# Optimization experiments

Measured on AMD Instinct MI355X. Metric: run time of the kernel, lower is better.

Reference implementation:

```python
import jax, jax.numpy as jnp
import numpy as np
import math

B, SQ, SKV, D = 16, 1024, 1024, 256


def setup_inputs() -> dict:
    key = jax.random.key(0)
    kq, kk, kv, km = jax.random.split(key, 4)
    # Scale inputs down: the module applies exp() to raw QK^T logits, so dot
    # products must stay small to avoid overflow (std ~ 0.05^2*sqrt(D) ~ 0.04).
    scale = 0.05
    query = jax.random.normal(kq, (B, SQ, D), dtype=jnp.float32) * scale
    key_t = jax.random.normal(kk, (B, SKV, D), dtype=jnp.float32) * scale
    value = jax.random.normal(kv, (B, SKV, D), dtype=jnp.float32)
    mask = jax.random.randint(km, (B, SQ, SKV), 0, 2, dtype=jnp.int32)
    return {"query": query, "key": key_t, "value": value, "mask": mask}


def reference(query, key, value, mask):
    # scores = exp(Q K^T) / sqrt(d)  -- note: exp BEFORE scaling, as in source
    d = query.shape[-1]
    inv_sqrt_d = jnp.float32(1.0 / math.sqrt(d))
    scores = jnp.exp(jnp.einsum('bqd,bkd->bqk', query, key)) * inv_sqrt_d
    # masked_fill(mask == 0, -1e9)
    scores = jnp.where(mask == 0, jnp.float32(-1e9), scores)
    p_attn = jax.nn.softmax(scores, axis=-1)
    # dropout is identity in eval mode (deterministic reference)
    output = jnp.einsum('bqk,bkd->bqd', p_attn, value)
    # flatten=True path: sum over the query/sequence dim
    return output.sum(axis=1), p_attn
```

## Files before the change

### kernel.cpp

```cpp
#include <hip/hip_runtime.h>

#define NB   16
#define NSQ  1024
#define NSKV 1024
#define ND   256

typedef __bf16    bf16x8 __attribute__((ext_vector_type(8)));
typedef float     f32x4  __attribute__((ext_vector_type(4)));
typedef _Float16  f16x4  __attribute__((ext_vector_type(4)));

#define EST 268

__global__ __launch_bounds__(256) void prep_kernel(
    const float* __restrict__ K, __bf16* __restrict__ Kbf,
    const int* __restrict__ mask, unsigned* __restrict__ mw,
    float* __restrict__ colsum, float* __restrict__ out0)
{
    const int bid = blockIdx.x;
    const int tid = threadIdx.x;
    if (bid < 2048) {
        const int i    = bid * 256 + tid;
        const int lane = i & 63;
        const int m    = lane & 15;
        const int kg   = lane >> 4;
        const int dc   = (i >> 6) & 7;
        const int kvb  = (i >> 9) & 63;
        const int b    = i >> 15;
        const float* s = K + ((size_t)(b * NSKV + kvb * 16 + m)) * ND + dc * 32 + kg * 8;
        float4 a = *(const float4*)s;
        float4 c = *(const float4*)(s + 4);
        bf16x8 o;
        o[0] = (__bf16)a.x; o[1] = (__bf16)a.y; o[2] = (__bf16)a.z; o[3] = (__bf16)a.w;
        o[4] = (__bf16)c.x; o[5] = (__bf16)c.y; o[6] = (__bf16)c.z; o[7] = (__bf16)c.w;
        ((bf16x8*)Kbf)[i] = o;
    } else if (bid < 2048 + 4096) {
        const int row = (bid - 2048) * 4 + (tid >> 6);
        const int l   = tid & 63;
        const int4* mrow = (const int4*)(mask + (size_t)row * NSKV) + l * 4;
        unsigned w = 0;
        #pragma unroll
        for (int v = 0; v < 4; ++v) {
            int4 mv = mrow[v];
            w |= (mv.x != 0 ? 1u : 0u) << (v * 4 + 0);
            w |= (mv.y != 0 ? 1u : 0u) << (v * 4 + 1);
            w |= (mv.z != 0 ? 1u : 0u) << (v * 4 + 2);
            w |= (mv.w != 0 ? 1u : 0u) << (v * 4 + 3);
        }
        const int m    = l & 15;
        const int base = l & 48;
        unsigned out = 0;
        #pragma unroll
        for (int c = 0; c < 16; ++c) {
            unsigned v = (unsigned)__shfl((int)w, base | c);
            out |= ((v >> m) & 1u) << c;
        }
        mw[(size_t)row * 64 + l] = out;
    } else if (bid < 2048 + 4096 + 64) {
        colsum[(bid - 6144) * 256 + tid] = 0.f;
    } else {
        out0[(bid - 6208) * 256 + tid] = 0.f;
    }
}

__global__ __launch_bounds__(256, 4) void attn_fused(
    const float* __restrict__ Q, const __bf16* __restrict__ Kbf,
    const unsigned* __restrict__ mw, float* __restrict__ out_p,
    float* __restrict__ colsum)
{
    const int b    = blockIdx.x >> 6;
    const int qt   = blockIdx.x & 63;
    const int q0   = qt * 16;
    const int tid  = threadIdx.x;
    const int lane = tid & 63;
    const int h    = tid >> 6;
    const int m    = lane & 15;
    const int kg   = lane >> 4;

    __shared__ __attribute__((aligned(16))) _Float16 epark[4][16 * EST];
    __shared__ float Zs[4][16];
    __shared__ float invZs[16];

    _Float16* myE = &epark[h][0];

    bf16x8 afrag[8];
    {
        const float* qbase = Q + ((size_t)(b * NSQ + q0 + m)) * ND;
        #pragma unroll
        for (int dc = 0; dc < 8; ++dc) {
            const float* p4 = qbase + dc * 32 + kg * 8;
            float4 x = *(const float4*)(p4);
            float4 y = *(const float4*)(p4 + 4);
            bf16x8 a;
            a[0] = (__bf16)x.x; a[1] = (__bf16)x.y; a[2] = (__bf16)x.z; a[3] = (__bf16)x.w;
            a[4] = (__bf16)y.x; a[5] = (__bf16)y.y; a[6] = (__bf16)y.z; a[7] = (__bf16)y.w;
            afrag[dc] = a;
        }
    }

    unsigned mword[4];
    #pragma unroll
    for (int i = 0; i < 4; ++i)
        mword[i] = mw[(size_t)(b * NSQ + q0 + kg * 4 + i) * 64 + h * 16 + m];

    const bf16x8* kf = (const bf16x8*)Kbf + ((size_t)(b * 64 + h * 16) * 8) * 64 + lane;

    float zacc[4] = {0.f, 0.f, 0.f, 0.f};
    bf16x8 fA[8], fB[8];

    #define LDFRAG(g, c) { \
        _Pragma("unroll") \
        for (int dc = 0; dc < 8; ++dc) \
            (g)[dc] = kf[((c) * 8 + dc) * 64]; }

    #define COMPUTE(g, c) { \
        f32x4 acc = {0.f, 0.f, 0.f, 0.f}; \
        _Pragma("unroll") \
        for (int dc = 0; dc < 8; ++dc) \
            acc = __builtin_amdgcn_mfma_f32_16x16x32_bf16(afrag[dc], (g)[dc], acc, 0, 0, 0); \
        _Pragma("unroll") \
        for (int i = 0; i < 4; ++i) { \
            float e = ((mword[i] >> (c)) & 1u) ? __expf(__expf(acc[i]) * 0.0625f) : 0.f; \
            zacc[i] += e; \
            myE[(kg * 4 + i) * EST + (c) * 16 + m] = (_Float16)e; \
        } }

    LDFRAG(fA, 0);

    #pragma unroll
    for (int cc = 0; cc < 16; cc += 2) {
        LDFRAG(fB, cc + 1);
        COMPUTE(fA, cc);
        if (cc + 2 < 16) LDFRAG(fA, cc + 2);
        COMPUTE(fB, cc + 1);
    }

    #pragma unroll
    for (int i = 0; i < 4; ++i) {
        float z = zacc[i];
        z += __shfl_xor(z, 1);
        z += __shfl_xor(z, 2);
        z += __shfl_xor(z, 4);
        z += __shfl_xor(z, 8);
        if (m == 0) Zs[h][kg * 4 + i] = z;
    }
    __syncthreads();
    if (tid < 16)
        invZs[tid] = 1.0f / (Zs[0][tid] + Zs[1][tid] + Zs[2][tid] + Zs[3][tid]);
    __syncthreads();

    float csum[4] = {0.f, 0.f, 0.f, 0.f};
    float* prow = out_p + (size_t)(b * NSQ + q0) * NSKV + h * 256 + lane * 4;
    #pragma unroll
    for (int s = 0; s < 16; ++s) {
        f16x4 ev = *(const f16x4*)&myE[s * EST + lane * 4];
        const float iz = invZs[s];
        float4 pv;
        pv.x = (float)ev[0] * iz; pv.y = (float)ev[1] * iz;
        pv.z = (float)ev[2] * iz; pv.w = (float)ev[3] * iz;
        *(float4*)(prow + (size_t)s * NSKV) = pv;
        csum[0] += pv.x; csum[1] += pv.y; csum[2] += pv.z; csum[3] += pv.w;
    }
    #pragma unroll
    for (int j = 0; j < 4; ++j)
        atomicAdd(&colsum[b * NSKV + h * 256 + lane * 4 + j], csum[j]);

    #undef LDFRAG
    #undef COMPUTE
}

__global__ __launch_bounds__(256) void attn_out_kernel(
    const float* __restrict__ colsum, const float* __restrict__ V,
    float* __restrict__ out)
{
    const int b  = blockIdx.x >> 6;
    const int ks = (blockIdx.x & 63) << 4;
    const int d  = threadIdx.x;
    float acc = 0.f;
    #pragma unroll
    for (int k = 0; k < 16; ++k) {
        acc += colsum[b * NSKV + ks + k] * V[((size_t)(b * NSKV + ks + k)) * ND + d];
    }
    atomicAdd(&out[b * ND + d], acc);
}

extern "C" void kernel_launch(void* const* d_in, const int* in_sizes, int n_in,
                              void* d_out, int out_size, void* d_ws, size_t ws_size,
                              hipStream_t stream)
{
    (void)in_sizes; (void)n_in; (void)out_size; (void)ws_size;
    const float* Q    = (const float*)d_in[0];
    const float* K    = (const float*)d_in[1];
    const float* V    = (const float*)d_in[2];
    const int*   mask = (const int*)d_in[3];

    float* out0 = (float*)d_out;
    float* p    = out0 + NB * ND;

    float*    colsum = (float*)d_ws;
    __bf16*   Kbf    = (__bf16*)((char*)d_ws + (64 << 10));
    unsigned* mwbits = (unsigned*)((char*)d_ws + (64 << 10) + (size_t)NB * NSKV * ND * 2);

    prep_kernel<<<6224, 256, 0, stream>>>(K, Kbf, mask, mwbits, colsum, out0);
    attn_fused<<<NB * 64, 256, 0, stream>>>(Q, Kbf, mwbits, p, colsum);
    attn_out_kernel<<<NB * 64, 256, 0, stream>>>(colsum, V, out0);
}
```

Baseline: 204.3 us.

## Make attention kernel persistent with LDS DMA K loads and deferred P stores

The fused attention kernel now runs 512 blocks that each process two query tiles. K fragments are streamed into double-buffered LDS through global_load_lds DMA, paced by explicit vmcnt waits. The previous tile's P rows are held in registers and written out interleaved with the next tile's DMA, so the global stores overlap compute. This aims to hide the K load latency and the large P write traffic, at the cost of higher register pressure (occupancy hint drops from 4 to 2 blocks) and fragile hand-written waitcnt ordering.

```diff
diff --git a/kernel.cpp b/kernel.cpp
--- a/kernel.cpp
+++ b/kernel.cpp
@@ -62,109 +62,149 @@
     }
 }
 
-__global__ __launch_bounds__(256, 4) void attn_fused(
+__device__ __forceinline__ void gload_lds16(const void* g, void* l) {
+    __builtin_amdgcn_global_load_lds(
+        (const __attribute__((address_space(1))) void*)g,
+        (__attribute__((address_space(3))) void*)l, 16, 0, 0);
+}
+
+__global__ __launch_bounds__(256, 2) void attn_fused(
     const float* __restrict__ Q, const __bf16* __restrict__ Kbf,
     const unsigned* __restrict__ mw, float* __restrict__ out_p,
     float* __restrict__ colsum)
 {
-    const int b    = blockIdx.x >> 6;
-    const int qt   = blockIdx.x & 63;
-    const int q0   = qt * 16;
     const int tid  = threadIdx.x;
     const int lane = tid & 63;
     const int h    = tid >> 6;
     const int m    = lane & 15;
     const int kg   = lane >> 4;
 
-    __shared__ __attribute__((aligned(16))) _Float16 epark[4][16 * EST];
+    __shared__ __attribute__((aligned(16))) char kbuf[4][2][8192];
     __shared__ float Zs[4][16];
     __shared__ float invZs[16];
 
-    _Float16* myE = &epark[h][0];
-
-    bf16x8 afrag[8];
-    {
-        const float* qbase = Q + ((size_t)(b * NSQ + q0 + m)) * ND;
-        #pragma unroll
-        for (int dc = 0; dc < 8; ++dc) {
-            const float* p4 = qbase + dc * 32 + kg * 8;
-            float4 x = *(const float4*)(p4);
-            float4 y = *(const float4*)(p4 + 4);
-            bf16x8 a;
-            a[0] = (__bf16)x.x; a[1] = (__bf16)x.y; a[2] = (__bf16)x.z; a[3] = (__bf16)x.w;
-            a[4] = (__bf16)y.x; a[5] = (__bf16)y.y; a[6] = (__bf16)y.z; a[7] = (__bf16)y.w;
-            afrag[dc] = a;
-        }
-    }
-
-    unsigned mword[4];
-    #pragma unroll
-    for (int i = 0; i < 4; ++i)
-        mword[i] = mw[(size_t)(b * NSQ + q0 + kg * 4 + i) * 64 + h * 16 + m];
-
-    const bf16x8* kf = (const bf16x8*)Kbf + ((size_t)(b * 64 + h * 16) * 8) * 64 + lane;
-
-    float zacc[4] = {0.f, 0.f, 0.f, 0.f};
-    bf16x8 fA[8], fB[8];
-
-    #define LDFRAG(g, c) { \
+    char* buf0 = &kbuf[h][0][0];
+    char* buf1 = &kbuf[h][1][0];
+    _Float16* myE = (_Float16*)buf0;
+
+    float4 pregs[16];
+    float* prow_prev = nullptr;
+
+    #define WAITVM(N) { asm volatile("s_waitcnt vmcnt(" #N ")" ::: "memory"); \
+                        __builtin_amdgcn_sched_barrier(0); }
+
+    #define DMA(bufp, c) { \
+        const char* _g = kf0 + (size_t)(c) * 8192; \
         _Pragma("unroll") \
-        for (int dc = 0; dc < 8; ++dc) \
-            (g)[dc] = kf[((c) * 8 + dc) * 64]; }
-
-    #define COMPUTE(g, c) { \
+        for (int j = 0; j < 8; ++j) \
+            gload_lds16(_g + j * 1024, (bufp) + j * 1024); }
+
+    #define COMPUTE(bufp, c) { \
         f32x4 acc = {0.f, 0.f, 0.f, 0.f}; \
         _Pragma("unroll") \
-        for (int dc = 0; dc < 8; ++dc) \
-            acc = __builtin_amdgcn_mfma_f32_16x16x32_bf16(afrag[dc], (g)[dc], acc, 0, 0, 0); \
+        for (int j = 0; j < 8; ++j) { \
+            bf16x8 bfr = *(const bf16x8*)((bufp) + j * 1024 + lane * 16); \
+            acc = __builtin_amdgcn_mfma_f32_16x16x32_bf16(afrag[j], bfr, acc, 0, 0, 0); \
+        } \
         _Pragma("unroll") \
         for (int i = 0; i < 4; ++i) { \
             float e = ((mword[i] >> (c)) & 1u) ? __expf(__expf(acc[i]) * 0.0625f) : 0.f; \
             zacc[i] += e; \
-            myE[(kg * 4 + i) * EST + (c) * 16 + m] = (_Float16)e; \
+            ebuf[c][i] = (_Float16)e; \
         } }
 
-    LDFRAG(fA, 0);
+    for (int t = 0; t < 2; ++t) {
+        const int tile = (int)blockIdx.x + t * 512;
+        const int b    = tile >> 6;
+        const int q0   = (tile & 63) * 16;
+        const bool prev = (t != 0);
+
+        bf16x8 afrag[8];
+        {
+            const float* qbase = Q + ((size_t)(b * NSQ + q0 + m)) * ND;
+            #pragma unroll
+            for (int dc = 0; dc < 8; ++dc) {
+                const float* p4 = qbase + dc * 32 + kg * 8;
+                float4 x = *(const float4*)(p4);
+                float4 y = *(const float4*)(p4 + 4);
+                bf16x8 a;
+                a[0] = (__bf16)x.x; a[1] = (__bf16)x.y; a[2] = (__bf16)x.z; a[3] = (__bf16)x.w;
+                a[4] = (__bf16)y.x; a[5] = (__bf16)y.y; a[6] = (__bf16)y.z; a[7] = (__bf16)y.w;
+                afrag[dc] = a;
+            }
+        }
+
+        unsigned mword[4];
+        #pragma unroll
+        for (int i = 0; i < 4; ++i)
+            mword[i] = mw[(size_t)(b * NSQ + q0 + kg * 4 + i) * 64 + h * 16 + m];
+
+        const char* kf0 = (const char*)Kbf
+                        + ((size_t)(b * 64 + h * 16) * 8 * 64) * 16 + lane * 16;
+
+        float zacc[4] = {0.f, 0.f, 0.f, 0.f};
+        f16x4 ebuf[16];
+
+        if (prev) *(float4*)(prow_prev + (size_t)0 * NSKV) = pregs[0];
+        DMA(buf0, 0);
+        if (prev) *(float4*)(prow_prev + (size_t)1 * NSKV) = pregs[1];
+        DMA(buf1, 1);
+
+        #pragma unroll
+        for (int cc = 0; cc < 16; ++cc) {
+            if (cc < 15) { WAITVM(8); } else { WAITVM(0); }
+            char* cbuf = (cc & 1) ? buf1 : buf0;
+            COMPUTE(cbuf, cc);
+            if (cc < 14) {
+                if (prev) *(float4*)(prow_prev + (size_t)(cc + 2) * NSKV) = pregs[cc + 2];
+                DMA(cbuf, cc + 2);
+            }
+        }
+
+        #pragma unroll
+        for (int c = 0; c < 16; ++c)
+            #pragma unroll
+            for (int i = 0; i < 4; ++i)
+                myE[(kg * 4 + i) * EST + c * 16 + m] = ebuf[c][i];
+
+        #pragma unroll
+        for (int i = 0; i < 4; ++i) {
+            float z = zacc[i];
+            z += __shfl_xor(z, 1);
+            z += __shfl_xor(z, 2);
+            z += __shfl_xor(z, 4);
+            z += __shfl_xor(z, 8);
+            if (m == 0) Zs[h][kg * 4 + i] = z;
+        }
+        __syncthreads();
+        if (tid < 16)
+            invZs[tid] = 1.0f / (Zs[0][tid] + Zs[1][tid] + Zs[2][tid] + Zs[3][tid]);
+        __syncthreads();
+
+        float csum[4] = {0.f, 0.f, 0.f, 0.f};
+        #pragma unroll
+        for (int s = 0; s < 16; ++s) {
+            f16x4 ev = *(const f16x4*)&myE[s * EST + lane * 4];
+            const float iz = invZs[s];
+            float4 pv;
+            pv.x = (float)ev[0] * iz; pv.y = (float)ev[1] * iz;
+            pv.z = (float)ev[2] * iz; pv.w = (float)ev[3] * iz;
+            pregs[s] = pv;
+            csum[0] += pv.x; csum[1] += pv.y; csum[2] += pv.z; csum[3] += pv.w;
+        }
+        #pragma unroll
+        for (int j = 0; j < 4; ++j)
+            atomicAdd(&colsum[b * NSKV + h * 256 + lane * 4 + j], csum[j]);
+
+        prow_prev = out_p + (size_t)(b * NSQ + q0) * NSKV + h * 256 + lane * 4;
+    }
 
     #pragma unroll
-    for (int cc = 0; cc < 16; cc += 2) {
-        LDFRAG(fB, cc + 1);
-        COMPUTE(fA, cc);
-        if (cc + 2 < 16) LDFRAG(fA, cc + 2);
-        COMPUTE(fB, cc + 1);
-    }
-
-    #pragma unroll
-    for (int i = 0; i < 4; ++i) {
-        float z = zacc[i];
-        z += __shfl_xor(z, 1);
-        z += __shfl_xor(z, 2);
-        z += __shfl_xor(z, 4);
-        z += __shfl_xor(z, 8);
-        if (m == 0) Zs[h][kg * 4 + i] = z;
-    }
-    __syncthreads();
-    if (tid < 16)
-        invZs[tid] = 1.0f / (Zs[0][tid] + Zs[1][tid] + Zs[2][tid] + Zs[3][tid]);
-    __syncthreads();
-
-    float csum[4] = {0.f, 0.f, 0.f, 0.f};
-    float* prow = out_p + (size_t)(b * NSQ + q0) * NSKV + h * 256 + lane * 4;
-    #pragma unroll
-    for (int s = 0; s < 16; ++s) {
-        f16x4 ev = *(const f16x4*)&myE[s * EST + lane * 4];
-        const float iz = invZs[s];
-        float4 pv;
-        pv.x = (float)ev[0] * iz; pv.y = (float)ev[1] * iz;
-        pv.z = (float)ev[2] * iz; pv.w = (float)ev[3] * iz;
-        *(float4*)(prow + (size_t)s * NSKV) = pv;
-        csum[0] += pv.x; csum[1] += pv.y; csum[2] += pv.z; csum[3] += pv.w;
-    }
-    #pragma unroll
-    for (int j = 0; j < 4; ++j)
-        atomicAdd(&colsum[b * NSKV + h * 256 + lane * 4 + j], csum[j]);
-
-    #undef LDFRAG
+    for (int s = 0; s < 16; ++s)
+        *(float4*)(prow_prev + (size_t)s * NSKV) = pregs[s];
+
+    #undef WAITVM
+    #undef DMA
     #undef COMPUTE
 }
 
@@ -201,6 +241,6 @@
     unsigned* mwbits = (unsigned*)((char*)d_ws + (64 << 10) + (size_t)NB * NSKV * ND * 2);
 
     prep_kernel<<<6224, 256, 0, stream>>>(K, Kbf, mask, mwbits, colsum, out0);
-    attn_fused<<<NB * 64, 256, 0, stream>>>(Q, Kbf, mwbits, p, colsum);
+    attn_fused<<<512, 256, 0, stream>>>(Q, Kbf, mwbits, p, colsum);
     attn_out_kernel<<<NB * 64, 256, 0, stream>>>(colsum, V, out0);
 }
```

Result: no change. 202.8 us (-0.7%).

## Split fused attention into a normalizer pass and a recompute-and-write pass

Applied to the files above, without the earlier changes.

The fused kernel is replaced by two kernels. The first computes only the row normalizers 1/Z and writes them to workspace. The second recomputes QK^T and the double exponential, then writes normalized probabilities straight from registers, with the column sums reduced by shuffles and atomics. This removes the large shared-memory staging buffer, which raises occupancy and drops the fp16 round-trip, and it adds a blockIdx swizzle meant to improve L2 locality. In exchange the MFMA and exp work runs twice, and the p stores become strided 4-byte scalar writes instead of float4 rows.

```diff
diff --git a/kernel.cpp b/kernel.cpp
--- a/kernel.cpp
+++ b/kernel.cpp
@@ -7,9 +7,6 @@
 
 typedef __bf16    bf16x8 __attribute__((ext_vector_type(8)));
 typedef float     f32x4  __attribute__((ext_vector_type(4)));
-typedef _Float16  f16x4  __attribute__((ext_vector_type(4)));
-
-#define EST 268
 
 __global__ __launch_bounds__(256) void prep_kernel(
     const float* __restrict__ K, __bf16* __restrict__ Kbf,
@@ -62,25 +59,21 @@
     }
 }
 
-__global__ __launch_bounds__(256, 4) void attn_fused(
+__global__ __launch_bounds__(256) void zed_kernel(
     const float* __restrict__ Q, const __bf16* __restrict__ Kbf,
-    const unsigned* __restrict__ mw, float* __restrict__ out_p,
-    float* __restrict__ colsum)
-{
-    const int b    = blockIdx.x >> 6;
-    const int qt   = blockIdx.x & 63;
-    const int q0   = qt * 16;
+    const unsigned* __restrict__ mw, float* __restrict__ invZ)
+{
+    const int g    = blockIdx.x;
+    const int tile = ((g & 7) << 7) | (g >> 3);
+    const int b    = tile >> 6;
+    const int q0   = (tile & 63) * 16;
     const int tid  = threadIdx.x;
     const int lane = tid & 63;
     const int h    = tid >> 6;
     const int m    = lane & 15;
     const int kg   = lane >> 4;
 
-    __shared__ __attribute__((aligned(16))) _Float16 epark[4][16 * EST];
     __shared__ float Zs[4][16];
-    __shared__ float invZs[16];
-
-    _Float16* myE = &epark[h][0];
 
     bf16x8 afrag[8];
     {
@@ -107,32 +100,32 @@
     float zacc[4] = {0.f, 0.f, 0.f, 0.f};
     bf16x8 fA[8], fB[8];
 
-    #define LDFRAG(g, c) { \
-        _Pragma("unroll") \
-        for (int dc = 0; dc < 8; ++dc) \
-            (g)[dc] = kf[((c) * 8 + dc) * 64]; }
-
-    #define COMPUTE(g, c) { \
+    #define LDFRAG(gr, c) { \
+        _Pragma("unroll") \
+        for (int dc = 0; dc < 8; ++dc) \
+            (gr)[dc] = kf[((c) * 8 + dc) * 64]; }
+
+    #define ZCOMP(gr, c) { \
         f32x4 acc = {0.f, 0.f, 0.f, 0.f}; \
         _Pragma("unroll") \
         for (int dc = 0; dc < 8; ++dc) \
-            acc = __builtin_amdgcn_mfma_f32_16x16x32_bf16(afrag[dc], (g)[dc], acc, 0, 0, 0); \
+            acc = __builtin_amdgcn_mfma_f32_16x16x32_bf16(afrag[dc], (gr)[dc], acc, 0, 0, 0); \
         _Pragma("unroll") \
         for (int i = 0; i < 4; ++i) { \
             float e = ((mword[i] >> (c)) & 1u) ? __expf(__expf(acc[i]) * 0.0625f) : 0.f; \
             zacc[i] += e; \
-            myE[(kg * 4 + i) * EST + (c) * 16 + m] = (_Float16)e; \
         } }
 
     LDFRAG(fA, 0);
-
     #pragma unroll
     for (int cc = 0; cc < 16; cc += 2) {
         LDFRAG(fB, cc + 1);
-        COMPUTE(fA, cc);
+        ZCOMP(fA, cc);
         if (cc + 2 < 16) LDFRAG(fA, cc + 2);
-        COMPUTE(fB, cc + 1);
-    }
+        ZCOMP(fB, cc + 1);
+    }
+    #undef LDFRAG
+    #undef ZCOMP
 
     #pragma unroll
     for (int i = 0; i < 4; ++i) {
@@ -145,27 +138,85 @@
     }
     __syncthreads();
     if (tid < 16)
-        invZs[tid] = 1.0f / (Zs[0][tid] + Zs[1][tid] + Zs[2][tid] + Zs[3][tid]);
-    __syncthreads();
-
-    float csum[4] = {0.f, 0.f, 0.f, 0.f};
-    float* prow = out_p + (size_t)(b * NSQ + q0) * NSKV + h * 256 + lane * 4;
-    #pragma unroll
-    for (int s = 0; s < 16; ++s) {
-        f16x4 ev = *(const f16x4*)&myE[s * EST + lane * 4];
-        const float iz = invZs[s];
-        float4 pv;
-        pv.x = (float)ev[0] * iz; pv.y = (float)ev[1] * iz;
-        pv.z = (float)ev[2] * iz; pv.w = (float)ev[3] * iz;
-        *(float4*)(prow + (size_t)s * NSKV) = pv;
-        csum[0] += pv.x; csum[1] += pv.y; csum[2] += pv.z; csum[3] += pv.w;
-    }
-    #pragma unroll
-    for (int j = 0; j < 4; ++j)
-        atomicAdd(&colsum[b * NSKV + h * 256 + lane * 4 + j], csum[j]);
-
+        invZ[b * NSQ + q0 + tid] = 1.0f / (Zs[0][tid] + Zs[1][tid] + Zs[2][tid] + Zs[3][tid]);
+}
+
+__global__ __launch_bounds__(256) void p_kernel(
+    const float* __restrict__ Q, const __bf16* __restrict__ Kbf,
+    const unsigned* __restrict__ mw, const float* __restrict__ invZ,
+    float* __restrict__ out_p, float* __restrict__ colsum)
+{
+    const int g    = blockIdx.x;
+    const int tile = ((g & 7) << 7) | (g >> 3);
+    const int b    = tile >> 6;
+    const int q0   = (tile & 63) * 16;
+    const int tid  = threadIdx.x;
+    const int lane = tid & 63;
+    const int h    = tid >> 6;
+    const int m    = lane & 15;
+    const int kg   = lane >> 4;
+
+    bf16x8 afrag[8];
+    {
+        const float* qbase = Q + ((size_t)(b * NSQ + q0 + m)) * ND;
+        #pragma unroll
+        for (int dc = 0; dc < 8; ++dc) {
+            const float* p4 = qbase + dc * 32 + kg * 8;
+            float4 x = *(const float4*)(p4);
+            float4 y = *(const float4*)(p4 + 4);
+            bf16x8 a;
+            a[0] = (__bf16)x.x; a[1] = (__bf16)x.y; a[2] = (__bf16)x.z; a[3] = (__bf16)x.w;
+            a[4] = (__bf16)y.x; a[5] = (__bf16)y.y; a[6] = (__bf16)y.z; a[7] = (__bf16)y.w;
+            afrag[dc] = a;
+        }
+    }
+
+    unsigned mword[4];
+    float    iz[4];
+    #pragma unroll
+    for (int i = 0; i < 4; ++i) {
+        mword[i] = mw[(size_t)(b * NSQ + q0 + kg * 4 + i) * 64 + h * 16 + m];
+        iz[i]    = invZ[b * NSQ + q0 + kg * 4 + i];
+    }
+
+    const bf16x8* kf = (const bf16x8*)Kbf + ((size_t)(b * 64 + h * 16) * 8) * 64 + lane;
+    float* pbase = out_p + (size_t)(b * NSQ + q0) * NSKV + h * 256 + m;
+    float* cbase = colsum + b * NSKV + h * 256 + m;
+
+    bf16x8 fA[8], fB[8];
+
+    #define LDFRAG(gr, c) { \
+        _Pragma("unroll") \
+        for (int dc = 0; dc < 8; ++dc) \
+            (gr)[dc] = kf[((c) * 8 + dc) * 64]; }
+
+    #define PCOMP(gr, c) { \
+        f32x4 acc = {0.f, 0.f, 0.f, 0.f}; \
+        _Pragma("unroll") \
+        for (int dc = 0; dc < 8; ++dc) \
+            acc = __builtin_amdgcn_mfma_f32_16x16x32_bf16(afrag[dc], (gr)[dc], acc, 0, 0, 0); \
+        float cs = 0.f; \
+        _Pragma("unroll") \
+        for (int i = 0; i < 4; ++i) { \
+            float e  = ((mword[i] >> (c)) & 1u) ? __expf(__expf(acc[i]) * 0.0625f) : 0.f; \
+            float pv = e * iz[i]; \
+            pbase[(size_t)(kg * 4 + i) * NSKV + (c) * 16] = pv; \
+            cs += pv; \
+        } \
+        cs += __shfl_xor(cs, 16); \
+        cs += __shfl_xor(cs, 32); \
+        if (kg == 0) atomicAdd(cbase + (c) * 16, cs); }
+
+    LDFRAG(fA, 0);
+    #pragma unroll
+    for (int cc = 0; cc < 16; cc += 2) {
+        LDFRAG(fB, cc + 1);
+        PCOMP(fA, cc);
+        if (cc + 2 < 16) LDFRAG(fA, cc + 2);
+        PCOMP(fB, cc + 1);
+    }
     #undef LDFRAG
-    #undef COMPUTE
+    #undef PCOMP
 }
 
 __global__ __launch_bounds__(256) void attn_out_kernel(
@@ -197,10 +248,12 @@
     float* p    = out0 + NB * ND;
 
     float*    colsum = (float*)d_ws;
-    __bf16*   Kbf    = (__bf16*)((char*)d_ws + (64 << 10));
-    unsigned* mwbits = (unsigned*)((char*)d_ws + (64 << 10) + (size_t)NB * NSKV * ND * 2);
+    float*    invZ   = (float*)((char*)d_ws + (64 << 10));
+    __bf16*   Kbf    = (__bf16*)((char*)d_ws + (128 << 10));
+    unsigned* mwbits = (unsigned*)((char*)d_ws + (128 << 10) + (size_t)NB * NSKV * ND * 2);
 
     prep_kernel<<<6224, 256, 0, stream>>>(K, Kbf, mask, mwbits, colsum, out0);
-    attn_fused<<<NB * 64, 256, 0, stream>>>(Q, Kbf, mwbits, p, colsum);
+    zed_kernel<<<NB * 64, 256, 0, stream>>>(Q, Kbf, mwbits, invZ);
+    p_kernel<<<NB * 64, 256, 0, stream>>>(Q, Kbf, mwbits, invZ, p, colsum);
     attn_out_kernel<<<NB * 64, 256, 0, stream>>>(colsum, V, out0);
 }
```

Measured after the change: 218.8 us. +7.1%, slower.

## Split attention into two-pass normalizer and probability kernels with LDS-staged K

Applied to the files above, without the earlier changes.

Replaces the single fused kernel, which parked f16 exp values in LDS and normalized afterward, with two kernels. The first computes only the row normalizers and writes 1/Z to workspace. The second recomputes QK^T and exp and writes normalized probabilities directly, with colsum atomics reduced across lanes first. Both stream K tiles into double-buffered LDS via global_load_lds DMA, with each workgroup covering 64 query rows so K is reused across more rows. This removes the f16 parking step and its LDS traffic, at the cost of doing the MFMA and exp work twice and launching fewer, larger blocks (256).

```diff
diff --git a/kernel.cpp b/kernel.cpp
--- a/kernel.cpp
+++ b/kernel.cpp
@@ -7,9 +7,6 @@
 
 typedef __bf16    bf16x8 __attribute__((ext_vector_type(8)));
 typedef float     f32x4  __attribute__((ext_vector_type(4)));
-typedef _Float16  f16x4  __attribute__((ext_vector_type(4)));
-
-#define EST 268
 
 __global__ __launch_bounds__(256) void prep_kernel(
     const float* __restrict__ K, __bf16* __restrict__ Kbf,
@@ -62,77 +59,101 @@
     }
 }
 
-__global__ __launch_bounds__(256, 4) void attn_fused(
+__device__ __forceinline__ void gload_lds16(const void* g, void* l) {
+    __builtin_amdgcn_global_load_lds(
+        (const __attribute__((address_space(1))) void*)g,
+        (__attribute__((address_space(3))) void*)l, 16, 0, 0);
+}
+
+
+#define PROLOGUE_COMMON \
+    const int g    = blockIdx.x; \
+    const int tile = ((g & 7) << 5) | (g >> 3); \
+    const int b    = tile >> 4; \
+    const int q0   = (tile & 15) * 64; \
+    const int tid  = threadIdx.x; \
+    const int lane = tid & 63; \
+    const int h    = tid >> 6; \
+    const int m    = lane & 15; \
+    const int kg   = lane >> 4; \
+    const int r0   = q0 + h * 16; \
+    bf16x8 afrag[8]; \
+    { \
+        const float* qbase = Q + ((size_t)(b * NSQ + r0 + m)) * ND; \
+        _Pragma("unroll") \
+        for (int dc = 0; dc < 8; ++dc) { \
+            const float* p4 = qbase + dc * 32 + kg * 8; \
+            float4 x = *(const float4*)(p4); \
+            float4 y = *(const float4*)(p4 + 4); \
+            bf16x8 a; \
+            a[0] = (__bf16)x.x; a[1] = (__bf16)x.y; a[2] = (__bf16)x.z; a[3] = (__bf16)x.w; \
+            a[4] = (__bf16)y.x; a[5] = (__bf16)y.y; a[6] = (__bf16)y.z; a[7] = (__bf16)y.w; \
+            afrag[dc] = a; \
+        } \
+    } \
+    unsigned long long mbits[4]; \
+    _Pragma("unroll") \
+    for (int i = 0; i < 4; ++i) { \
+        const unsigned* wp = mw + (size_t)(b * NSQ + r0 + kg * 4 + i) * 64 + m; \
+        unsigned long long w0 = wp[0], w1 = wp[16], w2 = wp[32], w3 = wp[48]; \
+        mbits[i] = w0 | (w1 << 16) | (w2 << 32) | (w3 << 48); \
+    } \
+    const char* ksrc = (const char*)Kbf + (size_t)b * 64 * 512 * 16; \
+    const int soff = h * 8192 + lane * 16; \
+    const int doff = h * 8192;
+
+#define DMA(c, dst) { \
+    const char* _g = ksrc + (size_t)(c) * 32768 + soff; \
+    char* _l = (dst) + doff; \
+    _Pragma("unroll") \
+    for (int j = 0; j < 8; ++j) \
+        gload_lds16(_g + j * 1024, _l + j * 1024); }
+
+#define SYNC(N) { asm volatile("s_waitcnt vmcnt(" #N ")" ::: "memory"); \
+                  __builtin_amdgcn_s_barrier(); \
+                  __builtin_amdgcn_sched_barrier(0); }
+
+__global__ __launch_bounds__(256) void zk_kernel(
     const float* __restrict__ Q, const __bf16* __restrict__ Kbf,
-    const unsigned* __restrict__ mw, float* __restrict__ out_p,
-    float* __restrict__ colsum)
-{
-    const int b    = blockIdx.x >> 6;
-    const int qt   = blockIdx.x & 63;
-    const int q0   = qt * 16;
-    const int tid  = threadIdx.x;
-    const int lane = tid & 63;
-    const int h    = tid >> 6;
-    const int m    = lane & 15;
-    const int kg   = lane >> 4;
-
-    __shared__ __attribute__((aligned(16))) _Float16 epark[4][16 * EST];
-    __shared__ float Zs[4][16];
-    __shared__ float invZs[16];
-
-    _Float16* myE = &epark[h][0];
-
-    bf16x8 afrag[8];
-    {
-        const float* qbase = Q + ((size_t)(b * NSQ + q0 + m)) * ND;
-        #pragma unroll
-        for (int dc = 0; dc < 8; ++dc) {
-            const float* p4 = qbase + dc * 32 + kg * 8;
-            float4 x = *(const float4*)(p4);
-            float4 y = *(const float4*)(p4 + 4);
-            bf16x8 a;
-            a[0] = (__bf16)x.x; a[1] = (__bf16)x.y; a[2] = (__bf16)x.z; a[3] = (__bf16)x.w;
-            a[4] = (__bf16)y.x; a[5] = (__bf16)y.y; a[6] = (__bf16)y.z; a[7] = (__bf16)y.w;
-            afrag[dc] = a;
-        }
-    }
-
-    unsigned mword[4];
-    #pragma unroll
-    for (int i = 0; i < 4; ++i)
-        mword[i] = mw[(size_t)(b * NSQ + q0 + kg * 4 + i) * 64 + h * 16 + m];
-
-    const bf16x8* kf = (const bf16x8*)Kbf + ((size_t)(b * 64 + h * 16) * 8) * 64 + lane;
-
+    const unsigned* __restrict__ mw, float* __restrict__ invZ)
+{
+    __shared__ __attribute__((aligned(16))) char kst[2][32768];
+    PROLOGUE_COMMON
+    char* b0 = &kst[0][0];
+    char* b1 = &kst[1][0];
     float zacc[4] = {0.f, 0.f, 0.f, 0.f};
-    bf16x8 fA[8], fB[8];
-
-    #define LDFRAG(g, c) { \
+
+    #define ZCOMP(cb, c) { \
         _Pragma("unroll") \
-        for (int dc = 0; dc < 8; ++dc) \
-            (g)[dc] = kf[((c) * 8 + dc) * 64]; }
-
-    #define COMPUTE(g, c) { \
-        f32x4 acc = {0.f, 0.f, 0.f, 0.f}; \
-        _Pragma("unroll") \
-        for (int dc = 0; dc < 8; ++dc) \
-            acc = __builtin_amdgcn_mfma_f32_16x16x32_bf16(afrag[dc], (g)[dc], acc, 0, 0, 0); \
-        _Pragma("unroll") \
-        for (int i = 0; i < 4; ++i) { \
-            float e = ((mword[i] >> (c)) & 1u) ? __expf(__expf(acc[i]) * 0.0625f) : 0.f; \
-            zacc[i] += e; \
-            myE[(kg * 4 + i) * EST + (c) * 16 + m] = (_Float16)e; \
+        for (int cs = 0; cs < 4; ++cs) { \
+            f32x4 acc = {0.f, 0.f, 0.f, 0.f}; \
+            _Pragma("unroll") \
+            for (int dc = 0; dc < 8; ++dc) { \
+                bf16x8 bfr = *(const bf16x8*)((cb) + cs * 8192 + dc * 1024 + lane * 16); \
+                acc = __builtin_amdgcn_mfma_f32_16x16x32_bf16(afrag[dc], bfr, acc, 0, 0, 0); \
+            } \
+            const int C_ = (c) * 4 + cs; \
+            _Pragma("unroll") \
+            for (int i = 0; i < 4; ++i) { \
+                float e = ((mbits[i] >> C_) & 1ull) ? __expf(__expf(acc[i]) * 0.0625f) : 0.f; \
+                zacc[i] += e; \
+            } \
         } }
 
-    LDFRAG(fA, 0);
-
-    #pragma unroll
-    for (int cc = 0; cc < 16; cc += 2) {
-        LDFRAG(fB, cc + 1);
-        COMPUTE(fA, cc);
-        if (cc + 2 < 16) LDFRAG(fA, cc + 2);
-        COMPUTE(fB, cc + 1);
-    }
+    DMA(0, b0);
+    SYNC(0);
+    DMA(1, b1);
+    for (int c = 0; c < 16; c += 2) {
+        ZCOMP(b0, c);
+        SYNC(0);
+        if (c + 2 < 16) DMA(c + 2, b0);
+        ZCOMP(b1, c + 1);
+        if (c + 2 < 16) {
+            SYNC(0);
+            DMA(c + 3, b1);
+        }
+    }
+    #undef ZCOMP
 
     #pragma unroll
     for (int i = 0; i < 4; ++i) {
@@ -141,31 +162,65 @@
         z += __shfl_xor(z, 2);
         z += __shfl_xor(z, 4);
         z += __shfl_xor(z, 8);
-        if (m == 0) Zs[h][kg * 4 + i] = z;
-    }
-    __syncthreads();
-    if (tid < 16)
-        invZs[tid] = 1.0f / (Zs[0][tid] + Zs[1][tid] + Zs[2][tid] + Zs[3][tid]);
-    __syncthreads();
-
-    float csum[4] = {0.f, 0.f, 0.f, 0.f};
-    float* prow = out_p + (size_t)(b * NSQ + q0) * NSKV + h * 256 + lane * 4;
+        if (m == 0) invZ[b * NSQ + r0 + kg * 4 + i] = 1.0f / z;
+    }
+}
+
+__global__ __launch_bounds__(256) void pk_kernel(
+    const float* __restrict__ Q, const __bf16* __restrict__ Kbf,
+    const unsigned* __restrict__ mw, const float* __restrict__ invZ,
+    float* __restrict__ out_p, float* __restrict__ colsum)
+{
+    __shared__ __attribute__((aligned(16))) char kst[2][32768];
+    PROLOGUE_COMMON
+    char* b0 = &kst[0][0];
+    char* b1 = &kst[1][0];
+
+    float iz[4];
     #pragma unroll
-    for (int s = 0; s < 16; ++s) {
-        f16x4 ev = *(const f16x4*)&myE[s * EST + lane * 4];
-        const float iz = invZs[s];
-        float4 pv;
-        pv.x = (float)ev[0] * iz; pv.y = (float)ev[1] * iz;
-        pv.z = (float)ev[2] * iz; pv.w = (float)ev[3] * iz;
-        *(float4*)(prow + (size_t)s * NSKV) = pv;
-        csum[0] += pv.x; csum[1] += pv.y; csum[2] += pv.z; csum[3] += pv.w;
-    }
-    #pragma unroll
-    for (int j = 0; j < 4; ++j)
-        atomicAdd(&colsum[b * NSKV + h * 256 + lane * 4 + j], csum[j]);
-
-    #undef LDFRAG
-    #undef COMPUTE
+    for (int i = 0; i < 4; ++i)
+        iz[i] = invZ[b * NSQ + r0 + kg * 4 + i];
+
+    float* pr0 = out_p + (size_t)(b * NSQ + r0 + kg * 4) * NSKV + m;
+    float* csb = colsum + b * NSKV + m;
+
+    #define PCOMP(cb, c) { \
+        _Pragma("unroll") \
+        for (int cs = 0; cs < 4; ++cs) { \
+            f32x4 acc = {0.f, 0.f, 0.f, 0.f}; \
+            _Pragma("unroll") \
+            for (int dc = 0; dc < 8; ++dc) { \
+                bf16x8 bfr = *(const bf16x8*)((cb) + cs * 8192 + dc * 1024 + lane * 16); \
+                acc = __builtin_amdgcn_mfma_f32_16x16x32_bf16(afrag[dc], bfr, acc, 0, 0, 0); \
+            } \
+            const int C_ = (c) * 4 + cs; \
+            float cssum = 0.f; \
+            _Pragma("unroll") \
+            for (int i = 0; i < 4; ++i) { \
+                float e  = ((mbits[i] >> C_) & 1ull) ? __expf(__expf(acc[i]) * 0.0625f) : 0.f; \
+                float pv = e * iz[i]; \
+                pr0[(size_t)i * NSKV + C_ * 16] = pv; \
+                cssum += pv; \
+            } \
+            cssum += __shfl_xor(cssum, 16); \
+            cssum += __shfl_xor(cssum, 32); \
+            if (kg == 0) atomicAdd(csb + C_ * 16, cssum); \
+        } }
+
+    DMA(0, b0);
+    SYNC(0);
+    DMA(1, b1);
+    for (int c = 0; c < 16; c += 2) {
+        PCOMP(b0, c);
+        SYNC(20);
+        if (c + 2 < 16) DMA(c + 2, b0);
+        PCOMP(b1, c + 1);
+        if (c + 2 < 16) {
+            SYNC(20);
+            DMA(c + 3, b1);
+        }
+    }
+    #undef PCOMP
 }
 
 __global__ __launch_bounds__(256) void attn_out_kernel(
@@ -197,10 +252,12 @@
     float* p    = out0 + NB * ND;
 
     float*    colsum = (float*)d_ws;
-    __bf16*   Kbf    = (__bf16*)((char*)d_ws + (64 << 10));
-    unsigned* mwbits = (unsigned*)((char*)d_ws + (64 << 10) + (size_t)NB * NSKV * ND * 2);
+    float*    invZ   = (float*)((char*)d_ws + (64 << 10));
+    __bf16*   Kbf    = (__bf16*)((char*)d_ws + (128 << 10));
+    unsigned* mwbits = (unsigned*)((char*)d_ws + (128 << 10) + (size_t)NB * NSKV * ND * 2);
 
     prep_kernel<<<6224, 256, 0, stream>>>(K, Kbf, mask, mwbits, colsum, out0);
-    attn_fused<<<NB * 64, 256, 0, stream>>>(Q, Kbf, mwbits, p, colsum);
+    zk_kernel<<<256, 256, 0, stream>>>(Q, Kbf, mwbits, invZ);
+    pk_kernel<<<256, 256, 0, stream>>>(Q, Kbf, mwbits, invZ, p, colsum);
     attn_out_kernel<<<NB * 64, 256, 0, stream>>>(colsum, V, out0);
 }
```

Measured after the change: 212.4 us. 4.0% more time.
